# Kernel tuning notes

Hardware: AMD Instinct MI355X
Metric: run time of the kernel (lower is better)

Reference implementation:

```python
import jax, jax.numpy as jnp
import numpy as np

N = 8388608          # number of samples (2**23)
T_MAX = 100000       # number of distinct time values -> ~84 ties per time


def setup_inputs() -> dict:
    key = jax.random.key(0)
    k1, k2, k3 = jax.random.split(key, 3)
    inp = jax.random.normal(k1, (N,), dtype=jnp.float32)            # log hazards
    target = jax.random.randint(k2, (N,), 0, T_MAX, dtype=jnp.int32)  # times
    weight = jax.random.randint(k3, (N,), 0, 2, dtype=jnp.int32)      # event indicator
    return {"input": inp, "target": target, "weight": weight}


def _cox_efron_npll(log_hz, time, event):
    """Negative Cox partial log-likelihood with Efron tie correction, mean reduction.

    Faithful to torchsurv's _partial_likelihood_efron: per unique time j,
    pll_j = sum_{i in H_j} log_hz_i - sum_{l=0}^{m_j-1} log(D_j - (l/m_j)*T_j)
    where H_j = events at time j, D_j = sum of exp(log_hz) over risk set (t>=t_j),
    T_j = sum of exp(log_hz) over H_j, m_j = |H_j|; loss = -mean over j with m_j>0.
    """
    n = log_hz.shape[0]
    order = jnp.argsort(time)                       # sort by time (group-sum math is tie-order invariant)
    t = time[order]
    lh = log_hz[order]
    ev = event[order].astype(lh.dtype)

    # group id per sample: 0..(num_unique-1), padded groups beyond that are empty
    new_grp = jnp.concatenate([jnp.zeros((1,), jnp.int32), (t[1:] != t[:-1]).astype(jnp.int32)])
    seg = jnp.cumsum(new_grp)                       # [n] int32

    hz = jnp.exp(lh)
    grp_hz = jax.ops.segment_sum(hz, seg, num_segments=n)          # sum exp per time group
    denom_naive = jnp.cumsum(grp_hz[::-1])[::-1]                   # risk-set sums (suffix over groups)
    m = jax.ops.segment_sum(ev, seg, num_segments=n)               # events per group
    log_nom = jax.ops.segment_sum(lh * ev, seg, num_segments=n)    # sum of log_hz over H_j
    ties = jax.ops.segment_sum(hz * ev, seg, num_segments=n)       # sum of exp over H_j

    # rank l in [0, m_j) of each event within its group
    csum_e = jnp.cumsum(ev)
    events_before = jnp.concatenate([jnp.zeros((1,), lh.dtype), jnp.cumsum(m)[:-1]])
    rank = csum_e - 1.0 - events_before[seg]
    mg = jnp.maximum(m[seg], 1.0)
    term = jnp.where(ev > 0.0,
                     jnp.log(denom_naive[seg] - (rank / mg) * ties[seg]),
                     0.0)
    log_denom = jax.ops.segment_sum(term, seg, num_segments=n)

    include = (m > 0.0).astype(lh.dtype)
    pll = jnp.where(m > 0.0, log_nom - log_denom, 0.0)
    # reduction='mean': -pll.nanmean() over groups that contain events
    return -(jnp.sum(pll) / jnp.sum(include))


def reference(input, target, weight):
    return _cox_efron_npll(input, target, weight)
```

## Files before the change

### kernel.cpp

```cpp
#include <hip/hip_runtime.h>

#define TMAXV 100000
#define CHUNK 256
#define NCHUNK ((TMAXV + CHUNK - 1) / CHUNK)
#define WB 512
#define LOGWB 9
#define SB ((TMAXV + WB - 1) / WB)
#define SBP 256
#define TILE 4096
#define RPT 16
#define KS 8
#define NREP 2
#define HSCALE 4096.0f
#define HINV (1.0f / 4096.0f)


__device__ __forceinline__ float block_reduce_sum(float v, float* sdata) {
    int lane = threadIdx.x & 63;
    int wid  = threadIdx.x >> 6;
    #pragma unroll
    for (int off = 32; off > 0; off >>= 1)
        v += __shfl_down(v, off, 64);
    if (lane == 0) sdata[wid] = v;
    __syncthreads();
    if (wid == 0) {
        v = (lane < 4) ? sdata[lane] : 0.0f;
        v += __shfl_down(v, 2, 64);
        v += __shfl_down(v, 1, 64);
    }
    return v;
}

__device__ __forceinline__ double block_reduce_sum_d(double v, double* sdata) {
    int lane = threadIdx.x & 63;
    int wid  = threadIdx.x >> 6;
    #pragma unroll
    for (int off = 32; off > 0; off >>= 1)
        v += __shfl_down(v, off, 64);
    if (lane == 0) sdata[wid] = v;
    __syncthreads();
    if (wid == 0) {
        v = (lane < 4) ? sdata[lane] : 0.0;
        v += __shfl_down(v, 2, 64);
        v += __shfl_down(v, 1, 64);
    }
    return v;
}

__device__ __forceinline__ unsigned encode_rec(float x, int t, int e) {
    float h = __expf(x);
    unsigned hf = (unsigned)__float2uint_rn(h * HSCALE);
    if (hf > 0x3FFFFFu) hf = 0x3FFFFFu;
    return (hf << 9)
         | (unsigned)(t & (WB - 1))
         | ((unsigned)e << 31);
}


__global__ void count_pfx_kernel(const int* __restrict__ tgt,
                                 int* __restrict__ pfx_arr,
                                 int* __restrict__ cnt_t,
                                 unsigned* __restrict__ zero_base,
                                 int nzero_dw, int n) {
    __shared__ int lc[SBP];
    __shared__ int ls[SBP];
    int tid = threadIdx.x, tile = blockIdx.x;
    for (int i = tile * 256 + tid; i < nzero_dw; i += gridDim.x * 256)
        zero_base[i] = 0u;
    lc[tid] = 0;
    __syncthreads();
    int lo = tile * TILE;
    if (lo + TILE <= n) {
        const int4* tgt4 = (const int4*)(tgt + lo);
        #pragma unroll
        for (int q = 0; q < RPT / 4; ++q) {
            int4 t4 = tgt4[q * 256 + tid];
            atomicAdd(&lc[t4.x >> LOGWB], 1);
            atomicAdd(&lc[t4.y >> LOGWB], 1);
            atomicAdd(&lc[t4.z >> LOGWB], 1);
            atomicAdd(&lc[t4.w >> LOGWB], 1);
        }
    } else {
        int hi = min(n, lo + TILE);
        for (int i = lo + tid; i < hi; i += 256)
            atomicAdd(&lc[tgt[i] >> LOGWB], 1);
    }
    __syncthreads();
    int c0 = lc[tid];
    ls[tid] = c0;
    __syncthreads();
    for (int off = 1; off < SBP; off <<= 1) {
        int a = (tid >= off) ? ls[tid - off] : 0;
        __syncthreads();
        ls[tid] += a;
        __syncthreads();
    }
    size_t rb = (size_t)tile * SBP;
    pfx_arr[rb + tid] = ls[tid] - c0;
    cnt_t[rb + tid] = c0;
}

__global__ void tile_scan_kernel(const int* __restrict__ cnt_t,
                                 int* __restrict__ tilebase_t,
                                 int* __restrict__ totals,
                                 int* __restrict__ base,
                                 unsigned* __restrict__ done,
                                 int nt, int n) {
    __shared__ int ls[256];
    __shared__ int lastFlag;
    int s = blockIdx.x, tid = threadIdx.x;
    int run = 0;
    for (int t0 = 0; t0 < nt; t0 += 256 * 8) {
        int c[8];
        #pragma unroll
        for (int u = 0; u < 8; ++u) {
            int t = t0 + tid * 8 + u;
            c[u] = (t < nt) ? cnt_t[(size_t)t * SBP + s] : 0;
        }
        int tot = 0;
        #pragma unroll
        for (int u = 0; u < 8; ++u) { int v = c[u]; c[u] = tot; tot += v; }
        ls[tid] = tot;
        __syncthreads();
        for (int off = 1; off < 256; off <<= 1) {
            int a = (tid >= off) ? ls[tid - off] : 0;
            __syncthreads();
            ls[tid] += a;
            __syncthreads();
        }
        int excl = ls[tid] - tot;
        int btot = ls[255];
        #pragma unroll
        for (int u = 0; u < 8; ++u) {
            int t = t0 + tid * 8 + u;
            if (t < nt) tilebase_t[(size_t)t * SBP + s] = run + excl + c[u];
        }
        run += btot;
        __syncthreads();
    }
    if (tid == 0) {
        __hip_atomic_store(&totals[s], run, __ATOMIC_RELEASE, __HIP_MEMORY_SCOPE_AGENT);
        unsigned prev = __hip_atomic_fetch_add(done, 1u, __ATOMIC_ACQ_REL, __HIP_MEMORY_SCOPE_AGENT);
        lastFlag = (prev == (unsigned)(gridDim.x - 1)) ? 1 : 0;
    }
    __syncthreads();
    if (lastFlag) {
        int c = __hip_atomic_load(&totals[tid], __ATOMIC_ACQUIRE, __HIP_MEMORY_SCOPE_AGENT);
        ls[tid] = c;
        __syncthreads();
        for (int off = 1; off < 256; off <<= 1) {
            int a = (tid >= off) ? ls[tid - off] : 0;
            __syncthreads();
            ls[tid] += a;
            __syncthreads();
        }
        base[tid] = ls[tid] - c;
        if (tid == 0) base[SBP] = n;
    }
}

__global__ void scatter_kernel(const float* __restrict__ lh,
                               const int*   __restrict__ tgt,
                               const int*   __restrict__ ev,
                               const int*   __restrict__ pfx_arr,
                               const int*   __restrict__ tilebase_t,
                               const int*   __restrict__ base,
                               unsigned* __restrict__ val,
                               double* __restrict__ acc, int n, int nt) {
    __shared__ unsigned fu[TILE];
    __shared__ unsigned char bidv[TILE];
    __shared__ int pfx[SBP];
    __shared__ int tb[SBP];
    __shared__ int lrank[SBP];
    __shared__ float sdata[4];
    int tid  = threadIdx.x;
    int tile = blockIdx.x;
    int lo   = tile * TILE;
    int cnt_here = min(TILE, n - lo);
    size_t rb = (size_t)tile * SBP;

    pfx[tid]   = pfx_arr[rb + tid];
    tb[tid]    = base[tid] + tilebase_t[rb + tid];
    lrank[tid] = 0;
    __syncthreads();

    float xl = 0.f;
    if (lo + TILE <= n) {
        const int4*   tgt4 = (const int4*)(tgt + lo);
        const int4*   ev4  = (const int4*)(ev + lo);
        const float4* lh4  = (const float4*)(lh + lo);
        #pragma unroll
        for (int q = 0; q < RPT / 4; ++q) {
            int idx = q * 256 + tid;
            int4   t4 = tgt4[idx];
            int4   e4 = ev4[idx];
            float4 x4 = lh4[idx];
            {
                int b = t4.x >> LOGWB; unsigned r = encode_rec(x4.x, t4.x, e4.x & 1);
                int k = atomicAdd(&lrank[b], 1); int pos = pfx[b] + k;
                fu[pos] = r; bidv[pos] = (unsigned char)b; if (e4.x & 1) xl += x4.x;
            }
            {
                int b = t4.y >> LOGWB; unsigned r = encode_rec(x4.y, t4.y, e4.y & 1);
                int k = atomicAdd(&lrank[b], 1); int pos = pfx[b] + k;
                fu[pos] = r; bidv[pos] = (unsigned char)b; if (e4.y & 1) xl += x4.y;
            }
            {
                int b = t4.z >> LOGWB; unsigned r = encode_rec(x4.z, t4.z, e4.z & 1);
                int k = atomicAdd(&lrank[b], 1); int pos = pfx[b] + k;
                fu[pos] = r; bidv[pos] = (unsigned char)b; if (e4.z & 1) xl += x4.z;
            }
            {
                int b = t4.w >> LOGWB; unsigned r = encode_rec(x4.w, t4.w, e4.w & 1);
                int k = atomicAdd(&lrank[b], 1); int pos = pfx[b] + k;
                fu[pos] = r; bidv[pos] = (unsigned char)b; if (e4.w & 1) xl += x4.w;
            }
        }
    } else {
        #pragma unroll
        for (int k = 0; k < RPT; ++k) {
            int i = lo + k * 256 + tid;
            if (i < n) {
                int t = tgt[i]; int e = ev[i] & 1; float x = lh[i];
                int b = t >> LOGWB; unsigned r = encode_rec(x, t, e);
                int rr = atomicAdd(&lrank[b], 1); int pos = pfx[b] + rr;
                fu[pos] = r; bidv[pos] = (unsigned char)b; if (e) xl += x;
            }
        }
    }
    __syncthreads();

    int pairs = cnt_here >> 1;
    const uint2* fu2 = (const uint2*)fu;
    for (int q = tid; q < pairs; q += 256) {
        uint2 bb = fu2[q];
        int p0 = q * 2;
        int b0 = (int)bidv[p0];
        int b1 = (int)bidv[p0 + 1];
        val[tb[b0] + (p0     - pfx[b0])] = bb.x;
        val[tb[b1] + (p0 + 1 - pfx[b1])] = bb.y;
    }
    if ((cnt_here & 1) && tid == 0) {
        int p = cnt_here - 1;
        int b = (int)bidv[p];
        val[tb[b] + (p - pfx[b])] = fu[p];
    }

    float rl = block_reduce_sum(xl, sdata);
    if (tid == 0) unsafeAtomicAdd(&acc[2], (double)rl);
}

__global__ void bucket_hist_kernel(const unsigned* __restrict__ val,
                                   const int* __restrict__ base,
                                   unsigned* __restrict__ sh_g,
                                   unsigned* __restrict__ cm_g,
                                   unsigned* __restrict__ th_g,
                                   float* __restrict__ chunk_sum) {
    __shared__ unsigned shi[NREP][WB];
    __shared__ unsigned cmi[NREP][WB];
    __shared__ unsigned thi[NREP][WB];
    __shared__ float sdata[4];
    __shared__ float sdata2[4];
    int tid = threadIdx.x;
    int rep = (tid >> 6) & (NREP - 1);
    int b   = blockIdx.x >> 3;
    int k   = blockIdx.x & (KS - 1);
    int lo0 = base[b], len = base[b + 1] - lo0;
    int lo  = lo0 + (int)(((long long)len * k) / KS);
    int hi  = lo0 + (int)(((long long)len * (k + 1)) / KS);

    #pragma unroll
    for (int u = 0; u < NREP * WB / 256; ++u) {
        ((unsigned*)shi)[u * 256 + tid] = 0u;
        ((unsigned*)cmi)[u * 256 + tid] = 0u;
        ((unsigned*)thi)[u * 256 + tid] = 0u;
    }
    __syncthreads();

    for (int i = lo + tid; i < hi; i += 256) {
        unsigned bits = val[i];
        int      s  = (int)(bits & (WB - 1));
        unsigned hf = (bits >> 9) & 0x3FFFFFu;
        atomicAdd(&shi[rep][s], hf);
        if (bits >> 31) {
            atomicAdd(&cmi[rep][s], 1u);
            atomicAdd(&thi[rep][s], hf);
        }
    }
    __syncthreads();

    unsigned s0 = shi[0][tid]       + shi[1][tid];
    unsigned s1 = shi[0][tid + 256] + shi[1][tid + 256];
    unsigned c0 = cmi[0][tid]       + cmi[1][tid];
    unsigned c1 = cmi[0][tid + 256] + cmi[1][tid + 256];
    unsigned t0v = thi[0][tid]       + thi[1][tid];
    unsigned t1v = thi[0][tid + 256] + thi[1][tid + 256];

    int t0 = b * WB + tid;
    if (s0)  atomicAdd(&sh_g[t0],       s0);
    if (s1)  atomicAdd(&sh_g[t0 + 256], s1);
    if (c0)  atomicAdd(&cm_g[t0],       c0);
    if (c1)  atomicAdd(&cm_g[t0 + 256], c1);
    if (t0v) atomicAdd(&th_g[t0],       t0v);
    if (t1v) atomicAdd(&th_g[t0 + 256], t1v);

    float r0 = block_reduce_sum((float)s0 * HINV, sdata);
    __syncthreads();
    float r1 = block_reduce_sum((float)s1 * HINV, sdata2);
    if (tid == 0) {
        unsafeAtomicAdd(&chunk_sum[2 * b],     r0);
        unsafeAtomicAdd(&chunk_sum[2 * b + 1], r1);
    }
}

__global__ void pll_suffix_kernel(const unsigned* __restrict__ sh_g,
                                  const unsigned* __restrict__ cm_g,
                                  const unsigned* __restrict__ th_g,
                                  const float* __restrict__ chunk_sum,
                                  double* __restrict__ acc,
                                  unsigned* __restrict__ done,
                                  float* __restrict__ out) {
    __shared__ float sf[CHUNK];
    __shared__ float sdata[4];
    __shared__ float sdata2[4];
    __shared__ double dsd[4];
    __shared__ double doff;
    int tid = threadIdx.x;
    int b   = blockIdx.x;
    int t   = b * CHUNK + tid;
    float sh = (float)sh_g[t] * HINV;
    unsigned cmu = cm_g[t];
    float th = (float)th_g[t] * HINV;
    sf[tid] = sh;
    __syncthreads();
    for (int off = 1; off < CHUNK; off <<= 1) {
        float add = (tid + off < CHUNK) ? sf[tid + off] : 0.0f;
        __syncthreads();
        sf[tid] += add;
        __syncthreads();
    }
    double mysum = 0.0;
    for (int j = b + 1 + tid; j < NCHUNK; j += 256)
        mysum += (double)chunk_sum[j];
    double red = block_reduce_sum_d(mysum, dsd);
    if (tid == 0) doff = red;
    __syncthreads();
    double off_d = doff;

    float pll = 0.0f, inc = 0.0f;
    if (t < TMAXV && cmu > 0u) {
        float cm   = (float)cmu;
        float D    = (float)(off_d + (double)sf[tid]);
        int   mi   = (int)cmu;
        float step = th / cm;
        float s = 0.0f;
        for (int l = 0; l < mi; ++l)
            s += __logf(D - (float)l * step);
        pll = -s;
        inc = 1.0f;
    }
    float rp = block_reduce_sum(pll, sdata);
    __syncthreads();
    float ri = block_reduce_sum(inc, sdata2);
    if (tid == 0) {
        unsafeAtomicAdd(&acc[0], (double)rp);
        unsafeAtomicAdd(&acc[1], (double)ri);
        __threadfence();
        unsigned prev = __hip_atomic_fetch_add(done, 1u, __ATOMIC_ACQ_REL, __HIP_MEMORY_SCOPE_AGENT);
        if (prev == (unsigned)(gridDim.x - 1)) {
            double a0 = __hip_atomic_load(&acc[0], __ATOMIC_ACQUIRE, __HIP_MEMORY_SCOPE_AGENT);
            double a1 = __hip_atomic_load(&acc[1], __ATOMIC_RELAXED, __HIP_MEMORY_SCOPE_AGENT);
            double a2 = __hip_atomic_load(&acc[2], __ATOMIC_RELAXED, __HIP_MEMORY_SCOPE_AGENT);
            out[0] = (a1 > 0.0) ? (float)(-(a0 + a2) / a1) : 0.0f;
        }
    }
}

__global__ void finalize_kernel(const double* __restrict__ acc,
                                float* __restrict__ out) {
    double cnt = acc[1];
    out[0] = (cnt > 0.0) ? (float)(-(acc[0] + acc[2]) / cnt) : 0.0f;
}

__global__ void hist_kernel(const float* __restrict__ lh,
                            const int*   __restrict__ tgt,
                            const int*   __restrict__ ev,
                            float* __restrict__ sum_hz,
                            float* __restrict__ mcnt,
                            float* __restrict__ log_nom,
                            float* __restrict__ ties,
                            int n) {
    int i = blockIdx.x * blockDim.x + threadIdx.x;
    if (i >= n) return;
    float x = lh[i];
    int   t = tgt[i];
    int   e = ev[i];
    float h = __expf(x);
    unsafeAtomicAdd(&sum_hz[t], h);
    if (e) {
        unsafeAtomicAdd(&mcnt[t], 1.0f);
        unsafeAtomicAdd(&log_nom[t], x);
        unsafeAtomicAdd(&ties[t], h);
    }
}

__global__ void chunk_sum_kernel(const float* __restrict__ sum_hz,
                                 float* __restrict__ chunk_sum) {
    __shared__ float sdata[4];
    int i = blockIdx.x * CHUNK + threadIdx.x;
    float v = (i < TMAXV) ? sum_hz[i] : 0.0f;
    v = block_reduce_sum(v, sdata);
    if (threadIdx.x == 0) chunk_sum[blockIdx.x] = v;
}

__global__ void chunk_scan_kernel(const float* __restrict__ chunk_sum,
                                  double* __restrict__ chunk_off) {
    __shared__ double ds[512];
    int tid = threadIdx.x;
    double own = (tid < NCHUNK) ? (double)chunk_sum[tid] : 0.0;
    ds[tid] = own;
    __syncthreads();
    for (int off = 1; off < 512; off <<= 1) {
        double add = (tid + off < 512) ? ds[tid + off] : 0.0;
        __syncthreads();
        ds[tid] += add;
        __syncthreads();
    }
    if (tid < NCHUNK) chunk_off[tid] = ds[tid] - own;
}

__global__ void pll_kernel(const float* __restrict__ mcnt,
                           const float* __restrict__ log_nom,
                           const float* __restrict__ ties,
                           const float* __restrict__ sum_hz,
                           const double* __restrict__ chunk_off,
                           double* __restrict__ acc) {
    __shared__ float sf[CHUNK];
    __shared__ float sdata[4];
    __shared__ float sdata2[4];
    int tid = threadIdx.x;
    int t   = blockIdx.x * CHUNK + tid;
    float v = (t < TMAXV) ? sum_hz[t] : 0.0f;
    sf[tid] = v;
    __syncthreads();
    for (int off = 1; off < CHUNK; off <<= 1) {
        float add = (tid + off < CHUNK) ? sf[tid + off] : 0.0f;
        __syncthreads();
        sf[tid] += add;
        __syncthreads();
    }
    float pll = 0.0f, inc = 0.0f;
    if (t < TMAXV) {
        float mv = mcnt[t];
        if (mv > 0.5f) {
            float D    = (float)(chunk_off[blockIdx.x] + (double)sf[tid]);
            float T    = ties[t];
            int   mi   = (int)(mv + 0.5f);
            float step = T / mv;
            float s = 0.0f;
            for (int l = 0; l < mi; ++l)
                s += __logf(D - (float)l * step);
            pll = log_nom[t] - s;
            inc = 1.0f;
        }
    }
    float rp = block_reduce_sum(pll, sdata);
    __syncthreads();
    float ri = block_reduce_sum(inc, sdata2);
    if (threadIdx.x == 0) {
        atomicAdd(&acc[0], (double)rp);
        atomicAdd(&acc[1], (double)ri);
    }
}

extern "C" void kernel_launch(void* const* d_in, const int* in_sizes, int n_in,
                              void* d_out, int out_size, void* d_ws, size_t ws_size,
                              hipStream_t stream) {
    const float* lh  = (const float*)d_in[0];
    const int*   tgt = (const int*)d_in[1];
    const int*   ev  = (const int*)d_in[2];
    float*       out = (float*)d_out;
    int n  = in_sizes[0];
    int nt = (n + TILE - 1) / TILE;

    char* ws = (char*)d_ws;
    size_t off = 0;
    auto take = [&](size_t bytes, size_t align) {
        off = (off + align - 1) & ~(align - 1);
        size_t r = off; off += bytes; return r;
    };
    size_t o_acc   = take(32, 16);
    size_t o_done  = take(16, 16);
    size_t o_csum  = take((size_t)512 * 4, 16);
    size_t o_shg   = take((size_t)SB * WB * 4, 16);
    size_t o_cmg   = take((size_t)SB * WB * 4, 16);
    size_t o_thg   = take((size_t)SB * WB * 4, 16);
    size_t zero_bytes = off;
    size_t o_base   = take((size_t)(SBP + 1) * 4, 16);
    size_t o_totals = take((size_t)SBP * 4, 16);
    size_t o_pfx    = take((size_t)nt * SBP * 4, 16);
    size_t o_cntt   = take((size_t)nt * SBP * 4, 16);
    size_t o_tbs    = take((size_t)nt * SBP * 4, 16);
    size_t o_val    = take((size_t)n * 4, 16);
    size_t need     = off;

    if (ws_size >= need) {
        double*   acc       = (double*)(ws + o_acc);
        unsigned* done      = (unsigned*)(ws + o_done);
        float*    chunk_sum = (float*)(ws + o_csum);
        unsigned* sh_g      = (unsigned*)(ws + o_shg);
        unsigned* cm_g      = (unsigned*)(ws + o_cmg);
        unsigned* th_g      = (unsigned*)(ws + o_thg);
        int*      base      = (int*)(ws + o_base);
        int*      totals    = (int*)(ws + o_totals);
        int*      pfx_arr   = (int*)(ws + o_pfx);
        int*      cnt_t     = (int*)(ws + o_cntt);
        int*      tilebase_t= (int*)(ws + o_tbs);
        unsigned* val       = (unsigned*)(ws + o_val);

        count_pfx_kernel<<<nt, 256, 0, stream>>>(tgt, pfx_arr, cnt_t,
                                                 (unsigned*)ws, (int)(zero_bytes / 4), n);
        tile_scan_kernel<<<SBP, 256, 0, stream>>>(cnt_t, tilebase_t, totals, base,
                                                  done + 0, nt, n);
        scatter_kernel<<<nt, 256, 0, stream>>>(lh, tgt, ev, pfx_arr, tilebase_t, base,
                                               val, acc, n, nt);
        bucket_hist_kernel<<<SB * KS, 256, 0, stream>>>(val, base, sh_g, cm_g, th_g,
                                                        chunk_sum);
        pll_suffix_kernel<<<NCHUNK, 256, 0, stream>>>(sh_g, cm_g, th_g, chunk_sum,
                                                      acc, done + 1, out);
    } else {
        size_t f = 0;
        auto ftake = [&](size_t bytes, size_t align) {
            f = (f + align - 1) & ~(align - 1);
            size_t r = f; f += bytes; return r;
        };
        size_t f_acc  = ftake(32, 16);
        size_t f_sum  = ftake((size_t)TMAXV * 4, 16);
        size_t f_m    = ftake((size_t)TMAXV * 4, 16);
        size_t f_ln   = ftake((size_t)TMAXV * 4, 16);
        size_t f_ties = ftake((size_t)TMAXV * 4, 16);
        size_t zb     = f;
        size_t f_csum = ftake((size_t)NCHUNK * 4, 16);
        size_t f_coff = ftake((size_t)NCHUNK * 8, 8);

        double* acc     = (double*)(ws + f_acc);
        float*  sum_hz  = (float*)(ws + f_sum);
        float*  mcnt    = (float*)(ws + f_m);
        float*  log_nom = (float*)(ws + f_ln);
        float*  ties    = (float*)(ws + f_ties);
        float*  chunk_sum = (float*)(ws + f_csum);
        double* chunk_off = (double*)(ws + f_coff);

        hipMemsetAsync(d_ws, 0, zb, stream);

        hist_kernel<<<(n + 255) / 256, 256, 0, stream>>>(lh, tgt, ev, sum_hz, mcnt, log_nom, ties, n);
        chunk_sum_kernel<<<NCHUNK, 256, 0, stream>>>(sum_hz, chunk_sum);
        chunk_scan_kernel<<<1, 512, 0, stream>>>(chunk_sum, chunk_off);
        pll_kernel<<<NCHUNK, 256, 0, stream>>>(mcnt, log_nom, ties, sum_hz, chunk_off, acc);
        finalize_kernel<<<1, 1, 0, stream>>>(acc, out);
    }
}
```

Before: 217.9 us.

## Fuse counting and scatter using per-bucket global atomic reservations into fixed-capacity slots

```diff
diff --git a/kernel.cpp b/kernel.cpp
--- a/kernel.cpp
+++ b/kernel.cpp
@@ -13,6 +13,7 @@
 #define NREP 2
 #define HSCALE 4096.0f
 #define HINV (1.0f / 4096.0f)
+#define CAPB 49152
 
 
 __device__ __forceinline__ float block_reduce_sum(float v, float* sdata) {
@@ -57,36 +58,50 @@
 }
 
 
-__global__ void count_pfx_kernel(const int* __restrict__ tgt,
-                                 int* __restrict__ pfx_arr,
-                                 int* __restrict__ cnt_t,
-                                 unsigned* __restrict__ zero_base,
-                                 int nzero_dw, int n) {
-    __shared__ int lc[SBP];
+__global__ void scatter_kernel(const float* __restrict__ lh,
+                               const int*   __restrict__ tgt,
+                               const int*   __restrict__ ev,
+                               int*      __restrict__ gcnt,
+                               unsigned* __restrict__ val,
+                               double*   __restrict__ acc,
+                               unsigned* __restrict__ zero_base,
+                               int nzero_dw, int n) {
+    __shared__ unsigned fu[TILE];
+    __shared__ unsigned char bidv[TILE];
+    __shared__ int cnl[SBP];
+    __shared__ int tb[SBP];
+    __shared__ int lrank[SBP];
     __shared__ int ls[SBP];
-    int tid = threadIdx.x, tile = blockIdx.x;
+    __shared__ float sdata[4];
+    int tid  = threadIdx.x;
+    int tile = blockIdx.x;
+
     for (int i = tile * 256 + tid; i < nzero_dw; i += gridDim.x * 256)
         zero_base[i] = 0u;
-    lc[tid] = 0;
-    __syncthreads();
+
+    cnl[tid] = 0; lrank[tid] = 0;
+    __syncthreads();
+
     int lo = tile * TILE;
+    int cnt_here = min(TILE, n - lo);
+
     if (lo + TILE <= n) {
         const int4* tgt4 = (const int4*)(tgt + lo);
         #pragma unroll
         for (int q = 0; q < RPT / 4; ++q) {
             int4 t4 = tgt4[q * 256 + tid];
-            atomicAdd(&lc[t4.x >> LOGWB], 1);
-            atomicAdd(&lc[t4.y >> LOGWB], 1);
-            atomicAdd(&lc[t4.z >> LOGWB], 1);
-            atomicAdd(&lc[t4.w >> LOGWB], 1);
+            atomicAdd(&cnl[t4.x >> LOGWB], 1);
+            atomicAdd(&cnl[t4.y >> LOGWB], 1);
+            atomicAdd(&cnl[t4.z >> LOGWB], 1);
+            atomicAdd(&cnl[t4.w >> LOGWB], 1);
         }
     } else {
-        int hi = min(n, lo + TILE);
-        for (int i = lo + tid; i < hi; i += 256)
-            atomicAdd(&lc[tgt[i] >> LOGWB], 1);
-    }
-    __syncthreads();
-    int c0 = lc[tid];
+        for (int i = lo + tid; i < lo + cnt_here; i += 256)
+            atomicAdd(&cnl[tgt[i] >> LOGWB], 1);
+    }
+    __syncthreads();
+
+    int c0 = cnl[tid];
     ls[tid] = c0;
     __syncthreads();
     for (int off = 1; off < SBP; off <<= 1) {
@@ -95,93 +110,14 @@
         ls[tid] += a;
         __syncthreads();
     }
-    size_t rb = (size_t)tile * SBP;
-    pfx_arr[rb + tid] = ls[tid] - c0;
-    cnt_t[rb + tid] = c0;
-}
-
-__global__ void tile_scan_kernel(const int* __restrict__ cnt_t,
-                                 int* __restrict__ tilebase_t,
-                                 int* __restrict__ totals,
-                                 int* __restrict__ base,
-                                 unsigned* __restrict__ done,
-                                 int nt, int n) {
-    __shared__ int ls[256];
-    __shared__ int lastFlag;
-    int s = blockIdx.x, tid = threadIdx.x;
-    int run = 0;
-    for (int t0 = 0; t0 < nt; t0 += 256 * 8) {
-        int c[8];
-        #pragma unroll
-        for (int u = 0; u < 8; ++u) {
-            int t = t0 + tid * 8 + u;
-            c[u] = (t < nt) ? cnt_t[(size_t)t * SBP + s] : 0;
-        }
-        int tot = 0;
-        #pragma unroll
-        for (int u = 0; u < 8; ++u) { int v = c[u]; c[u] = tot; tot += v; }
-        ls[tid] = tot;
-        __syncthreads();
-        for (int off = 1; off < 256; off <<= 1) {
-            int a = (tid >= off) ? ls[tid - off] : 0;
-            __syncthreads();
-            ls[tid] += a;
-            __syncthreads();
-        }
-        int excl = ls[tid] - tot;
-        int btot = ls[255];
-        #pragma unroll
-        for (int u = 0; u < 8; ++u) {
-            int t = t0 + tid * 8 + u;
-            if (t < nt) tilebase_t[(size_t)t * SBP + s] = run + excl + c[u];
-        }
-        run += btot;
-        __syncthreads();
-    }
-    if (tid == 0) {
-        __hip_atomic_store(&totals[s], run, __ATOMIC_RELEASE, __HIP_MEMORY_SCOPE_AGENT);
-        unsigned prev = __hip_atomic_fetch_add(done, 1u, __ATOMIC_ACQ_REL, __HIP_MEMORY_SCOPE_AGENT);
-        lastFlag = (prev == (unsigned)(gridDim.x - 1)) ? 1 : 0;
-    }
-    __syncthreads();
-    if (lastFlag) {
-        int c = __hip_atomic_load(&totals[tid], __ATOMIC_ACQUIRE, __HIP_MEMORY_SCOPE_AGENT);
-        ls[tid] = c;
-        __syncthreads();
-        for (int off = 1; off < 256; off <<= 1) {
-            int a = (tid >= off) ? ls[tid - off] : 0;
-            __syncthreads();
-            ls[tid] += a;
-            __syncthreads();
-        }
-        base[tid] = ls[tid] - c;
-        if (tid == 0) base[SBP] = n;
-    }
-}
-
-__global__ void scatter_kernel(const float* __restrict__ lh,
-                               const int*   __restrict__ tgt,
-                               const int*   __restrict__ ev,
-                               const int*   __restrict__ pfx_arr,
-                               const int*   __restrict__ tilebase_t,
-                               const int*   __restrict__ base,
-                               unsigned* __restrict__ val,
-                               double* __restrict__ acc, int n, int nt) {
-    __shared__ unsigned fu[TILE];
-    __shared__ unsigned char bidv[TILE];
-    __shared__ int pfx[SBP];
-    __shared__ int tb[SBP];
-    __shared__ int lrank[SBP];
-    __shared__ float sdata[4];
-    int tid  = threadIdx.x;
-    int tile = blockIdx.x;
-    int lo   = tile * TILE;
-    int cnt_here = min(TILE, n - lo);
-    size_t rb = (size_t)tile * SBP;
-
-    pfx[tid]   = pfx_arr[rb + tid];
-    tb[tid]    = base[tid] + tilebase_t[rb + tid];
-    lrank[tid] = 0;
+    int pfxv = ls[tid] - c0;
+    int res = 0;
+    if (c0 > 0) {
+        res = atomicAdd(&gcnt[tid * 16], c0);
+        if (res > CAPB) res = CAPB;
+    }
+    cnl[tid] = pfxv;
+    tb[tid]  = tid * CAPB + res - pfxv;
     __syncthreads();
 
     float xl = 0.f;
@@ -197,35 +133,31 @@
             float4 x4 = lh4[idx];
             {
                 int b = t4.x >> LOGWB; unsigned r = encode_rec(x4.x, t4.x, e4.x & 1);
-                int k = atomicAdd(&lrank[b], 1); int pos = pfx[b] + k;
+                int k = atomicAdd(&lrank[b], 1); int pos = cnl[b] + k;
                 fu[pos] = r; bidv[pos] = (unsigned char)b; if (e4.x & 1) xl += x4.x;
             }
             {
                 int b = t4.y >> LOGWB; unsigned r = encode_rec(x4.y, t4.y, e4.y & 1);
-                int k = atomicAdd(&lrank[b], 1); int pos = pfx[b] + k;
+                int k = atomicAdd(&lrank[b], 1); int pos = cnl[b] + k;
                 fu[pos] = r; bidv[pos] = (unsigned char)b; if (e4.y & 1) xl += x4.y;
             }
             {
                 int b = t4.z >> LOGWB; unsigned r = encode_rec(x4.z, t4.z, e4.z & 1);
-                int k = atomicAdd(&lrank[b], 1); int pos = pfx[b] + k;
+                int k = atomicAdd(&lrank[b], 1); int pos = cnl[b] + k;
                 fu[pos] = r; bidv[pos] = (unsigned char)b; if (e4.z & 1) xl += x4.z;
             }
             {
                 int b = t4.w >> LOGWB; unsigned r = encode_rec(x4.w, t4.w, e4.w & 1);
-                int k = atomicAdd(&lrank[b], 1); int pos = pfx[b] + k;
+                int k = atomicAdd(&lrank[b], 1); int pos = cnl[b] + k;
                 fu[pos] = r; bidv[pos] = (unsigned char)b; if (e4.w & 1) xl += x4.w;
             }
         }
     } else {
-        #pragma unroll
-        for (int k = 0; k < RPT; ++k) {
-            int i = lo + k * 256 + tid;
-            if (i < n) {
-                int t = tgt[i]; int e = ev[i] & 1; float x = lh[i];
-                int b = t >> LOGWB; unsigned r = encode_rec(x, t, e);
-                int rr = atomicAdd(&lrank[b], 1); int pos = pfx[b] + rr;
-                fu[pos] = r; bidv[pos] = (unsigned char)b; if (e) xl += x;
-            }
+        for (int i = lo + tid; i < lo + cnt_here; i += 256) {
+            int t = tgt[i]; int e = ev[i] & 1; float x = lh[i];
+            int b = t >> LOGWB; unsigned r = encode_rec(x, t, e);
+            int rr = atomicAdd(&lrank[b], 1); int pos = cnl[b] + rr;
+            fu[pos] = r; bidv[pos] = (unsigned char)b; if (e) xl += x;
         }
     }
     __syncthreads();
@@ -237,13 +169,13 @@
         int p0 = q * 2;
         int b0 = (int)bidv[p0];
         int b1 = (int)bidv[p0 + 1];
-        val[tb[b0] + (p0     - pfx[b0])] = bb.x;
-        val[tb[b1] + (p0 + 1 - pfx[b1])] = bb.y;
+        val[tb[b0] + p0]     = bb.x;
+        val[tb[b1] + p0 + 1] = bb.y;
     }
     if ((cnt_here & 1) && tid == 0) {
         int p = cnt_here - 1;
         int b = (int)bidv[p];
-        val[tb[b] + (p - pfx[b])] = fu[p];
+        val[tb[b] + p] = fu[p];
     }
 
     float rl = block_reduce_sum(xl, sdata);
@@ -251,7 +183,7 @@
 }
 
 __global__ void bucket_hist_kernel(const unsigned* __restrict__ val,
-                                   const int* __restrict__ base,
+                                   const int* __restrict__ gcnt,
                                    unsigned* __restrict__ sh_g,
                                    unsigned* __restrict__ cm_g,
                                    unsigned* __restrict__ th_g,
@@ -265,7 +197,8 @@
     int rep = (tid >> 6) & (NREP - 1);
     int b   = blockIdx.x >> 3;
     int k   = blockIdx.x & (KS - 1);
-    int lo0 = base[b], len = base[b + 1] - lo0;
+    int len = gcnt[b * 16]; if (len > CAPB) len = CAPB;
+    int lo0 = b * CAPB;
     int lo  = lo0 + (int)(((long long)len * k) / KS);
     int hi  = lo0 + (int)(((long long)len * (k + 1)) / KS);
 
@@ -490,44 +423,36 @@
         size_t r = off; off += bytes; return r;
     };
     size_t o_acc   = take(32, 16);
+    size_t o_gcnt  = take((size_t)SB * 64, 64);
+    size_t zero1   = off;
     size_t o_done  = take(16, 16);
     size_t o_csum  = take((size_t)512 * 4, 16);
     size_t o_shg   = take((size_t)SB * WB * 4, 16);
     size_t o_cmg   = take((size_t)SB * WB * 4, 16);
     size_t o_thg   = take((size_t)SB * WB * 4, 16);
-    size_t zero_bytes = off;
-    size_t o_base   = take((size_t)(SBP + 1) * 4, 16);
-    size_t o_totals = take((size_t)SBP * 4, 16);
-    size_t o_pfx    = take((size_t)nt * SBP * 4, 16);
-    size_t o_cntt   = take((size_t)nt * SBP * 4, 16);
-    size_t o_tbs    = take((size_t)nt * SBP * 4, 16);
-    size_t o_val    = take((size_t)n * 4, 16);
-    size_t need     = off;
-
-    if (ws_size >= need) {
+    size_t zero2_end = off;
+    size_t o_val   = take((size_t)(SB + 1) * CAPB * 4, 16);
+    size_t need    = off;
+
+    if (ws_size >= need && n <= 9000000) {
         double*   acc       = (double*)(ws + o_acc);
+        int*      gcnt      = (int*)(ws + o_gcnt);
         unsigned* done      = (unsigned*)(ws + o_done);
         float*    chunk_sum = (float*)(ws + o_csum);
         unsigned* sh_g      = (unsigned*)(ws + o_shg);
         unsigned* cm_g      = (unsigned*)(ws + o_cmg);
         unsigned* th_g      = (unsigned*)(ws + o_thg);
-        int*      base      = (int*)(ws + o_base);
-        int*      totals    = (int*)(ws + o_totals);
-        int*      pfx_arr   = (int*)(ws + o_pfx);
-        int*      cnt_t     = (int*)(ws + o_cntt);
-        int*      tilebase_t= (int*)(ws + o_tbs);
         unsigned* val       = (unsigned*)(ws + o_val);
 
-        count_pfx_kernel<<<nt, 256, 0, stream>>>(tgt, pfx_arr, cnt_t,
-                                                 (unsigned*)ws, (int)(zero_bytes / 4), n);
-        tile_scan_kernel<<<SBP, 256, 0, stream>>>(cnt_t, tilebase_t, totals, base,
-                                                  done + 0, nt, n);
-        scatter_kernel<<<nt, 256, 0, stream>>>(lh, tgt, ev, pfx_arr, tilebase_t, base,
-                                               val, acc, n, nt);
-        bucket_hist_kernel<<<SB * KS, 256, 0, stream>>>(val, base, sh_g, cm_g, th_g,
+        hipMemsetAsync(ws, 0, zero1, stream);
+
+        scatter_kernel<<<nt, 256, 0, stream>>>(lh, tgt, ev, gcnt, val, acc,
+                                               (unsigned*)(ws + o_done),
+                                               (int)((zero2_end - o_done) / 4), n);
+        bucket_hist_kernel<<<SB * KS, 256, 0, stream>>>(val, gcnt, sh_g, cm_g, th_g,
                                                         chunk_sum);
         pll_suffix_kernel<<<NCHUNK, 256, 0, stream>>>(sh_g, cm_g, th_g, chunk_sum,
-                                                      acc, done + 1, out);
+                                                      acc, done, out);
     } else {
         size_t f = 0;
         auto ftake = [&](size_t bytes, size_t align) {
```

Measured after the change: 216.1 us. Within noise of the previous version (-0.8%).

## Pad per-tile bucket segments to multiples of four for 128-bit scatter and histogram loads

Applied to the files above, without the earlier changes.

```diff
diff --git a/kernel.cpp b/kernel.cpp
--- a/kernel.cpp
+++ b/kernel.cpp
@@ -13,6 +13,7 @@
 #define NREP 2
 #define HSCALE 4096.0f
 #define HINV (1.0f / 4096.0f)
+#define FUSZ (TILE + 640)
 
 
 __device__ __forceinline__ float block_reduce_sum(float v, float* sdata) {
@@ -60,6 +61,7 @@
 __global__ void count_pfx_kernel(const int* __restrict__ tgt,
                                  int* __restrict__ pfx_arr,
                                  int* __restrict__ cnt_t,
+                                 int* __restrict__ tot_t,
                                  unsigned* __restrict__ zero_base,
                                  int nzero_dw, int n) {
     __shared__ int lc[SBP];
@@ -86,8 +88,8 @@
             atomicAdd(&lc[tgt[i] >> LOGWB], 1);
     }
     __syncthreads();
-    int c0 = lc[tid];
-    ls[tid] = c0;
+    int cp = (lc[tid] + 3) & ~3;
+    ls[tid] = cp;
     __syncthreads();
     for (int off = 1; off < SBP; off <<= 1) {
         int a = (tid >= off) ? ls[tid - off] : 0;
@@ -96,8 +98,9 @@
         __syncthreads();
     }
     size_t rb = (size_t)tile * SBP;
-    pfx_arr[rb + tid] = ls[tid] - c0;
-    cnt_t[rb + tid] = c0;
+    pfx_arr[rb + tid] = ls[tid] - cp;
+    cnt_t[rb + tid] = cp;
+    if (tid == 255) tot_t[tile] = ls[255];
 }
 
 __global__ void tile_scan_kernel(const int* __restrict__ cnt_t,
@@ -155,7 +158,7 @@
             __syncthreads();
         }
         base[tid] = ls[tid] - c;
-        if (tid == 0) base[SBP] = n;
+        if (tid == 255) base[SBP] = ls[255];
     }
 }
 
@@ -165,13 +168,15 @@
                                const int*   __restrict__ pfx_arr,
                                const int*   __restrict__ tilebase_t,
                                const int*   __restrict__ base,
+                               const int*   __restrict__ tot_t,
                                unsigned* __restrict__ val,
                                double* __restrict__ acc, int n, int nt) {
-    __shared__ unsigned fu[TILE];
-    __shared__ unsigned char bidv[TILE];
+    __shared__ alignas(16) unsigned fu[FUSZ];
+    __shared__ unsigned char bidv[FUSZ];
     __shared__ int pfx[SBP];
     __shared__ int tb[SBP];
     __shared__ int lrank[SBP];
+    __shared__ int stot;
     __shared__ float sdata[4];
     int tid  = threadIdx.x;
     int tile = blockIdx.x;
@@ -182,6 +187,7 @@
     pfx[tid]   = pfx_arr[rb + tid];
     tb[tid]    = base[tid] + tilebase_t[rb + tid];
     lrank[tid] = 0;
+    if (tid == 0) stot = tot_t[tile];
     __syncthreads();
 
     float xl = 0.f;
@@ -217,33 +223,30 @@
             }
         }
     } else {
-        #pragma unroll
-        for (int k = 0; k < RPT; ++k) {
-            int i = lo + k * 256 + tid;
-            if (i < n) {
-                int t = tgt[i]; int e = ev[i] & 1; float x = lh[i];
-                int b = t >> LOGWB; unsigned r = encode_rec(x, t, e);
-                int rr = atomicAdd(&lrank[b], 1); int pos = pfx[b] + rr;
-                fu[pos] = r; bidv[pos] = (unsigned char)b; if (e) xl += x;
-            }
-        }
-    }
-    __syncthreads();
-
-    int pairs = cnt_here >> 1;
-    const uint2* fu2 = (const uint2*)fu;
-    for (int q = tid; q < pairs; q += 256) {
-        uint2 bb = fu2[q];
-        int p0 = q * 2;
-        int b0 = (int)bidv[p0];
-        int b1 = (int)bidv[p0 + 1];
-        val[tb[b0] + (p0     - pfx[b0])] = bb.x;
-        val[tb[b1] + (p0 + 1 - pfx[b1])] = bb.y;
-    }
-    if ((cnt_here & 1) && tid == 0) {
-        int p = cnt_here - 1;
-        int b = (int)bidv[p];
-        val[tb[b] + (p - pfx[b])] = fu[p];
+        for (int i = lo + tid; i < lo + cnt_here; i += 256) {
+            int t = tgt[i]; int e = ev[i] & 1; float x = lh[i];
+            int b = t >> LOGWB; unsigned r = encode_rec(x, t, e);
+            int rr = atomicAdd(&lrank[b], 1); int pos = pfx[b] + rr;
+            fu[pos] = r; bidv[pos] = (unsigned char)b; if (e) xl += x;
+        }
+    }
+    __syncthreads();
+
+    {
+        int pb = pfx[tid] + lrank[tid];
+        int pe = ((tid == 255) ? stot : pfx[tid + 1]);
+        for (int p = pb; p < pe; ++p) fu[p] = 0u;
+    }
+    __syncthreads();
+
+    int groups = stot >> 2;
+    const uint4* fu4 = (const uint4*)fu;
+    uint4* val4 = (uint4*)val;
+    for (int g = tid; g < groups; g += 256) {
+        uint4 bb = fu4[g];
+        int p0 = g * 4;
+        int b  = (int)bidv[p0];
+        val4[(tb[b] + p0 - pfx[b]) >> 2] = bb;
     }
 
     float rl = block_reduce_sum(xl, sdata);
@@ -266,8 +269,8 @@
     int b   = blockIdx.x >> 3;
     int k   = blockIdx.x & (KS - 1);
     int lo0 = base[b], len = base[b + 1] - lo0;
-    int lo  = lo0 + (int)(((long long)len * k) / KS);
-    int hi  = lo0 + (int)(((long long)len * (k + 1)) / KS);
+    int li  = lo0 + ((int)(((long long)len * k) / KS) & ~3);
+    int hi  = lo0 + ((int)(((long long)len * (k + 1)) / KS) & ~3);
 
     #pragma unroll
     for (int u = 0; u < NREP * WB / 256; ++u) {
@@ -277,16 +280,21 @@
     }
     __syncthreads();
 
-    for (int i = lo + tid; i < hi; i += 256) {
-        unsigned bits = val[i];
-        int      s  = (int)(bits & (WB - 1));
-        unsigned hf = (bits >> 9) & 0x3FFFFFu;
-        atomicAdd(&shi[rep][s], hf);
-        if (bits >> 31) {
-            atomicAdd(&cmi[rep][s], 1u);
-            atomicAdd(&thi[rep][s], hf);
-        }
-    }
+    const uint4* v4 = (const uint4*)val;
+#define HPROC(bits)                                                        \
+    {                                                                      \
+        unsigned _b = (bits);                                              \
+        int      _s = (int)(_b & (WB - 1));                                \
+        unsigned _h = (_b >> 9) & 0x3FFFFFu;                               \
+        atomicAdd(&shi[rep][_s], _h);                                      \
+        if (_b >> 31) { atomicAdd(&cmi[rep][_s], 1u);                      \
+                        atomicAdd(&thi[rep][_s], _h); }                    \
+    }
+    for (int g = (li >> 2) + tid; g < (hi >> 2); g += 256) {
+        uint4 w = v4[g];
+        HPROC(w.x); HPROC(w.y); HPROC(w.z); HPROC(w.w);
+    }
+#undef HPROC
     __syncthreads();
 
     unsigned s0 = shi[0][tid]       + shi[1][tid];
@@ -498,10 +506,10 @@
     size_t zero_bytes = off;
     size_t o_base   = take((size_t)(SBP + 1) * 4, 16);
     size_t o_totals = take((size_t)SBP * 4, 16);
+    size_t o_tot    = take((size_t)nt * 4, 16);
     size_t o_pfx    = take((size_t)nt * SBP * 4, 16);
-    size_t o_cntt   = take((size_t)nt * SBP * 4, 16);
     size_t o_tbs    = take((size_t)nt * SBP * 4, 16);
-    size_t o_val    = take((size_t)n * 4, 16);
+    size_t o_val    = take((size_t)(n + 3 * (size_t)nt * SB + 64) * 4, 16);
     size_t need     = off;
 
     if (ws_size >= need) {
@@ -513,17 +521,18 @@
         unsigned* th_g      = (unsigned*)(ws + o_thg);
         int*      base      = (int*)(ws + o_base);
         int*      totals    = (int*)(ws + o_totals);
+        int*      tot_t     = (int*)(ws + o_tot);
         int*      pfx_arr   = (int*)(ws + o_pfx);
-        int*      cnt_t     = (int*)(ws + o_cntt);
         int*      tilebase_t= (int*)(ws + o_tbs);
+        int*      cnt_t     = (int*)(ws + o_val);
         unsigned* val       = (unsigned*)(ws + o_val);
 
-        count_pfx_kernel<<<nt, 256, 0, stream>>>(tgt, pfx_arr, cnt_t,
+        count_pfx_kernel<<<nt, 256, 0, stream>>>(tgt, pfx_arr, cnt_t, tot_t,
                                                  (unsigned*)ws, (int)(zero_bytes / 4), n);
         tile_scan_kernel<<<SBP, 256, 0, stream>>>(cnt_t, tilebase_t, totals, base,
                                                   done + 0, nt, n);
         scatter_kernel<<<nt, 256, 0, stream>>>(lh, tgt, ev, pfx_arr, tilebase_t, base,
-                                               val, acc, n, nt);
+                                               tot_t, val, acc, n, nt);
         bucket_hist_kernel<<<SB * KS, 256, 0, stream>>>(val, base, sh_g, cm_g, th_g,
                                                         chunk_sum);
         pll_suffix_kernel<<<NCHUNK, 256, 0, stream>>>(sh_g, cm_g, th_g, chunk_sum,
```

New measurement: 218.6 us. No clear change (+0.3%).
